# Performance work log

Hardware: AMD Instinct MI355X
Metric: run time of the kernel (lower is better)

Reference implementation:

```python
import jax, jax.numpy as jnp
import numpy as np

B, T, C, H = 2, 2048, 1024, 16
DH = C // H  # 64


def setup_inputs() -> dict:
    key = jax.random.key(0)
    ks = jax.random.split(key, 8)
    scale = 1.0 / np.sqrt(C)
    x = jax.random.normal(ks[0], (B, T, C), dtype=jnp.float32)
    mask = jax.random.randint(ks[1], (B, T), 0, 2, dtype=jnp.int32)
    Wq = jax.random.normal(ks[2], (C, C), dtype=jnp.float32) * scale
    bq = jnp.zeros((C,), dtype=jnp.float32)
    Wk = jax.random.normal(ks[3], (C, C), dtype=jnp.float32) * scale
    bk = jnp.zeros((C,), dtype=jnp.float32)
    Wv = jax.random.normal(ks[4], (C, C), dtype=jnp.float32) * scale
    bv = jnp.zeros((C,), dtype=jnp.float32)
    return {"x": x, "Wq": Wq, "bq": bq, "Wk": Wk, "bk": bk, "Wv": Wv, "bv": bv, "mask": mask}


def reference(x, Wq, bq, Wk, bk, Wv, bv, mask):
    # q/k/v projections: [B,T,C] -> [B,H,T,DH]
    def proj(W, b):
        return (x @ W + b).reshape(B, T, H, DH).transpose(0, 2, 1, 3)

    q = proj(Wq, bq)
    k = proj(Wk, bk)
    v = proj(Wv, bv)

    att = jnp.einsum("bhqd,bhkd->bhqk", q, k) * (1.0 / np.sqrt(DH))

    # outer-product padding mask: square_mask[b,q,k] = mask[b,q]*mask[b,k]
    m = mask.astype(jnp.float32)
    square_mask = m[:, :, None] * m[:, None, :]           # [B,T,T]
    sm = (square_mask != 0)[:, None, :, :]                 # [B,1,T,T]
    att = jnp.where(sm, att, -jnp.inf)

    # rows that are fully masked (query token padded) -> softmax gives NaN
    # in torch; torch then zeros the NaNs. Replicate with a safe softmax.
    row_valid = (mask != 0)[:, None, :, None]              # [B,1,T,1]
    att_safe = jnp.where(row_valid, att, 0.0)
    att = jax.nn.softmax(att_safe, axis=-1)
    att = jnp.where(row_valid, att, 0.0)
    # attn_pdrop = 0.0 -> dropout is identity

    y = jnp.einsum("bhqk,bhkd->bhqd", att, v)              # [B,H,T,DH]
    y = y.transpose(0, 2, 1, 3).reshape(B, T, C)
    return y
```

## Files before the change

### kernel.cpp

```cpp
#include <hip/hip_runtime.h>

#define B_ 2
#define T_ 2048
#define C_ 1024
#define H_ 16
#define DH_ 64

typedef __attribute__((ext_vector_type(8))) _Float16 half8;
typedef __attribute__((ext_vector_type(4))) _Float16 half4;
typedef __attribute__((ext_vector_type(2))) __fp16 fp16x2;
typedef __attribute__((ext_vector_type(4))) float f32x4;
typedef __attribute__((ext_vector_type(16))) float f32x16;

__device__ __forceinline__ unsigned short f2h(float f) {
    union { _Float16 h; unsigned short u; } cv; cv.h = (_Float16)f; return cv.u;
}
__device__ __forceinline__ unsigned pk2(float a, float b) {
    union { fp16x2 h; unsigned u; } cv;
    cv.h = __builtin_amdgcn_cvt_pkrtz(a, b);
    return cv.u;
}
__device__ __forceinline__ void plswap(unsigned &a, unsigned &b) {
    asm volatile("v_permlane32_swap_b32 %0, %1" : "+v"(a), "+v"(b));
}

__device__ __forceinline__ void gll16(const void* g, void* l) {
    __builtin_amdgcn_global_load_lds(
        (const __attribute__((address_space(1))) void*)g,
        (__attribute__((address_space(3))) void*)l, 16, 0, 0);
}

__global__ __launch_bounds__(256) void prep_kernel(
    const float* __restrict__ x, unsigned short* __restrict__ xf,
    const int* __restrict__ mask, unsigned short* __restrict__ mb,
    const float* __restrict__ Wq, const float* __restrict__ Wk,
    const float* __restrict__ Wv, unsigned short* __restrict__ wt)
{
    __shared__ float tile[32][33];
    const int tid = threadIdx.x;

    if (blockIdx.x < 2048) {
        const size_t idx8 = ((size_t)blockIdx.x * 256 + tid) * 8;
        float4 v0 = *(const float4*)(x + idx8);
        float4 v1 = *(const float4*)(x + idx8 + 4);
        float f[8] = {v0.x, v0.y, v0.z, v0.w, v1.x, v1.y, v1.z, v1.w};
        unsigned short h[8];
#pragma unroll
        for (int i = 0; i < 8; i++) h[i] = f2h(f[i]);
        *(uint4*)(xf + idx8) = *(const uint4*)h;

        if (blockIdx.x == 0) {
#pragma unroll
            for (int j = 0; j < 16; j++) {
                int i = tid * 16 + j;
                mb[i] = (mask[i] != 0) ? (unsigned short)0x3C00 : (unsigned short)0;
            }
        }
    } else {
        const int idx = blockIdx.x - 2048;
        const int z   = idx >> 10;
        const int rem = idx & 1023;
        const int n0  = (rem & 31) * 32;
        const int k0  = (rem >> 5) * 32;
        const float* __restrict__ W = (z == 0) ? Wq : (z == 1) ? Wk : Wv;
        unsigned short* __restrict__ wtz = wt + (size_t)z * C_ * C_;
        const int tx = tid & 31;
        const int ty = tid >> 5;
#pragma unroll
        for (int j = 0; j < 4; j++)
            tile[ty + j * 8][tx] = W[(size_t)(k0 + ty + j * 8) * C_ + n0 + tx];
        __syncthreads();
#pragma unroll
        for (int j = 0; j < 4; j++)
            wtz[(size_t)(n0 + ty + j * 8) * C_ + k0 + tx] = f2h(tile[tx][ty + j * 8]);
    }
}

__global__ __launch_bounds__(256) void qkv_mfma_kernel(
    const unsigned short* __restrict__ xf, const unsigned short* __restrict__ wt,
    const float* __restrict__ bq, const float* __restrict__ bk,
    const float* __restrict__ bv, const int* __restrict__ maskp,
    unsigned short* __restrict__ qb, unsigned short* __restrict__ kb,
    unsigned short* __restrict__ vt)
{
    __shared__ unsigned short sX[128 * 64];
    __shared__ unsigned short sW[128 * 64];

    const int bid  = blockIdx.x;
    const int virt = (bid & 7) * 96 + (bid >> 3);
    const int yz   = virt >> 5;
    const int tokb = virt & 31;
    const int z    = yz >> 3;
    const int yb   = yz & 7;

    const float* __restrict__ bias = (z == 0) ? bq : (z == 1) ? bk : bv;
    const unsigned short* __restrict__ wtz = wt + (size_t)z * C_ * C_;

    const int tok0 = tokb * 128;
    const int col0 = yb * 128;
    const int wv    = threadIdx.x >> 6;
    const int lane  = threadIdx.x & 63;
    const int l15   = lane & 15;
    const int quad  = lane >> 4;
    const int l7    = l15 & 7;
    const int wm    = wv >> 1;
    const int wn    = wv & 1;
    const int lrow8 = lane >> 3;
    const int gch   = (lane & 7) ^ lrow8;

    f32x4 acc[4][4];
#pragma unroll
    for (int i = 0; i < 4; i++)
#pragma unroll
        for (int j = 0; j < 4; j++) acc[i][j] = (f32x4){0.f, 0.f, 0.f, 0.f};

    int aoff[4][2], boff[4][2];
#pragma unroll
    for (int i = 0; i < 4; i++)
#pragma unroll
        for (int s = 0; s < 2; s++) {
            aoff[i][s] = (wm * 64 + i * 16 + l15) * 64 + (((s * 4 + quad) ^ l7) * 8);
            boff[i][s] = (wn * 64 + i * 16 + l15) * 64 + (((s * 4 + quad) ^ l7) * 8);
        }

    const unsigned short* Abuf = (z < 2) ? sX : sW;
    const unsigned short* Bbuf = (z < 2) ? sW : sX;

    for (int k0 = 0; k0 < C_; k0 += 64) {
        __syncthreads();
#pragma unroll
        for (int s = 0; s < 8; ++s) {
            int g    = (s << 2) + wv;
            int tsel = g >> 4;
            int r0   = (g & 15) << 3;
            const unsigned short* src = tsel ? wtz : xf;
            unsigned short*       dst = tsel ? sW  : sX;
            int rowg = tsel ? col0 : tok0;
            gll16(src + (size_t)(rowg + r0 + lrow8) * C_ + k0 + gch * 8,
                  dst + r0 * 64);
        }
        __syncthreads();

        half8 af[4][2], bf_[4][2];
#pragma unroll
        for (int i = 0; i < 4; i++)
#pragma unroll
            for (int s = 0; s < 2; s++) {
                af[i][s]  = *(const half8*)&Abuf[aoff[i][s]];
                bf_[i][s] = *(const half8*)&Bbuf[boff[i][s]];
            }
#pragma unroll
        for (int s = 0; s < 2; s++)
#pragma unroll
            for (int j = 0; j < 4; j++)
#pragma unroll
                for (int i = 0; i < 4; i++)
                    acc[i][j] = __builtin_amdgcn_mfma_f32_16x16x32_f16(
                        af[i][s], bf_[j][s], acc[i][j], 0, 0, 0);
    }

    if (z == 0) {
#pragma unroll
        for (int j = 0; j < 4; j++) {
            int col = col0 + wn * 64 + j * 16 + l15;
            int h = col >> 6, d = col & 63;
            float bs = bias[col];
#pragma unroll
            for (int i = 0; i < 4; i++) {
#pragma unroll
                for (int r = 0; r < 4; r++) {
                    int tok = tok0 + wm * 64 + i * 16 + quad * 4 + r;
                    int bidx = tok >> 11, t = tok & (T_ - 1);
                    qb[((size_t)(bidx * H_ + h) * T_ + t) * DH_ + d] =
                        f2h((acc[i][j][r] + bs) * 0.18033688011112042f);
                }
            }
        }
    } else if (z == 1) {
#pragma unroll
        for (int j = 0; j < 4; j++) {
            int col = col0 + wn * 64 + j * 16 + l15;
            int h = col >> 6, d = col & 63;
            float bs = bias[col];
#pragma unroll
            for (int i = 0; i < 4; i++) {
#pragma unroll
                for (int r = 0; r < 4; r++) {
                    int tok = tok0 + wm * 64 + i * 16 + quad * 4 + r;
                    int bidx = tok >> 11, t = tok & (T_ - 1);
                    kb[((size_t)(bidx * H_ + h) * T_ + t) * DH_ + d] =
                        f2h(acc[i][j][r] + bs);
                }
            }
        }
    } else {
        float mv4[4]; int bidx4[4], t4[4];
#pragma unroll
        for (int j = 0; j < 4; j++) {
            int tok = tok0 + wn * 64 + j * 16 + l15;
            bidx4[j] = tok >> 11; t4[j] = tok & (T_ - 1);
            mv4[j] = (maskp[bidx4[j] * T_ + t4[j]] != 0) ? 1.f : 0.f;
        }
#pragma unroll
        for (int i = 0; i < 4; i++) {
#pragma unroll
            for (int r = 0; r < 4; r++) {
                int col = col0 + wm * 64 + i * 16 + quad * 4 + r;
                int h = col >> 6, d = col & 63;
                float bs = bias[col];
#pragma unroll
                for (int j = 0; j < 4; j++) {
                    vt[((size_t)(bidx4[j] * H_ + h) * DH_ + d) * T_ + t4[j]] =
                        f2h((acc[i][j][r] + bs) * mv4[j]);
                }
            }
        }
    }
}

__global__ __launch_bounds__(256, 2) void attn_mfma_kernel(
    const unsigned short* __restrict__ qb,
    const unsigned short* __restrict__ kb,
    const unsigned short* __restrict__ vt,
    const int* __restrict__ mask,
    const unsigned short* __restrict__ mb,
    float* __restrict__ out)
{
    __shared__ unsigned short Ks[2][64 * 64];
    __shared__ unsigned short Vs[2][64 * 64];

    const int bh   = blockIdx.x;
    const int b    = bh >> 4;
    const int h    = bh & 15;
    const int wv   = threadIdx.x >> 6;
    const int lane = threadIdx.x & 63;
    const int l31  = lane & 31;
    const int hi   = lane >> 5;
    const int l7b  = l31 & 7;
    const int q0w  = blockIdx.y * 128 + wv * 32;

    const unsigned short* kbh = kb + (size_t)bh * T_ * DH_;
    const unsigned short* vbh = vt + (size_t)bh * DH_ * T_;
    const unsigned short* mbb = mb + b * T_;
    const int* __restrict__ mrow = mask + b * T_;

    half8 qf[4];
#pragma unroll
    for (int m = 0; m < 4; ++m)
        qf[m] = *(const half8*)(qb + ((size_t)bh * T_ + q0w + l31) * DH_
                                + m * 16 + hi * 8);

    f32x16 o0, o1, lacc;
#pragma unroll
    for (int r = 0; r < 16; ++r) { o0[r] = 0.f; o1[r] = 0.f; lacc[r] = 0.f; }

    const int lrow = lane >> 3;
    const int gch  = (lane & 7) ^ lrow;

#pragma unroll
    for (int s = 0; s < 4; ++s) {
        int j  = (wv << 2) + s;
        int rb = j & 7;
        if (j < 8) gll16(kbh + (size_t)(rb * 8 + lrow) * DH_ + gch * 8, &Ks[0][rb * 512]);
        else       gll16(vbh + (size_t)(rb * 8 + lrow) * T_  + gch * 8, &Vs[0][rb * 512]);
    }

    for (int kt = 0; kt < 32; ++kt) {
        const int cur   = kt & 1;
        const int kbase = kt * 64;
        __syncthreads();

        if (kt < 31) {
            const int nb = kbase + 64;
#pragma unroll
            for (int s = 0; s < 4; ++s) {
                int j  = (wv << 2) + s;
                int rb = j & 7;
                if (j < 8) gll16(kbh + (size_t)(nb + rb * 8 + lrow) * DH_ + gch * 8,
                                 &Ks[cur ^ 1][rb * 512]);
                else       gll16(vbh + (size_t)(rb * 8 + lrow) * T_ + nb + gch * 8,
                                 &Vs[cur ^ 1][rb * 512]);
            }
        }

        const unsigned short* Kc = &Ks[cur][0];
        const unsigned short* Vc = &Vs[cur][0];

        half8 bm[4];
#pragma unroll
        for (int c = 0; c < 4; ++c)
            bm[c] = *(const half8*)(mbb + kbase + c * 16 + hi * 8);

        half8 pa[4];
#pragma unroll
        for (int st = 0; st < 2; ++st) {
            f32x16 sa;
#pragma unroll
            for (int r = 0; r < 16; ++r) sa[r] = 0.f;
#pragma unroll
            for (int m = 0; m < 4; ++m) {
                half8 kf = *(const half8*)(Kc + (st * 32 + l31) * 64
                                           + (((m * 2 + hi) ^ l7b) * 8));
                sa = __builtin_amdgcn_mfma_f32_32x32x16_f16(kf, qf[m], sa, 0, 0, 0);
            }
            float p[16];
#pragma unroll
            for (int r = 0; r < 16; ++r) p[r] = __builtin_amdgcn_exp2f(sa[r]);
#pragma unroll
            for (int kh = 0; kh < 2; ++kh) {
                unsigned w0 = pk2(p[kh * 8 + 0], p[kh * 8 + 1]);
                unsigned w2 = pk2(p[kh * 8 + 4], p[kh * 8 + 5]);
                unsigned w1 = pk2(p[kh * 8 + 2], p[kh * 8 + 3]);
                unsigned w3 = pk2(p[kh * 8 + 6], p[kh * 8 + 7]);
                plswap(w0, w2);
                plswap(w1, w3);
                union { unsigned u[4]; half8 hh; } cv;
                cv.u[0] = w0; cv.u[1] = w1; cv.u[2] = w2; cv.u[3] = w3;
                pa[st * 2 + kh] = cv.hh;
            }
        }

#pragma unroll
        for (int c = 0; c < 4; ++c)
            lacc = __builtin_amdgcn_mfma_f32_32x32x16_f16(pa[c], bm[c], lacc, 0, 0, 0);

#pragma unroll
        for (int c = 0; c < 4; ++c) {
            half8 v0 = *(const half8*)(Vc + (l31) * 64      + (((c * 2 + hi) ^ l7b) * 8));
            half8 v1 = *(const half8*)(Vc + (32 + l31) * 64 + (((c * 2 + hi) ^ l7b) * 8));
            o0 = __builtin_amdgcn_mfma_f32_32x32x16_f16(pa[c], v0, o0, 0, 0, 0);
            o1 = __builtin_amdgcn_mfma_f32_32x32x16_f16(pa[c], v1, o1, 0, 0, 0);
        }
    }

#pragma unroll
    for (int r = 0; r < 16; ++r) {
        int q = q0w + (r & 3) + 8 * (r >> 2) + 4 * hi;
        float lv = lacc[r];
        float iv = (mrow[q] != 0 && lv > 0.f) ? (1.0f / lv) : 0.f;
        float* orow = out + ((size_t)(b * T_ + q)) * C_ + h * DH_;
        orow[l31]      = o0[r] * iv;
        orow[32 + l31] = o1[r] * iv;
    }
}

extern "C" void kernel_launch(void* const* d_in, const int* in_sizes, int n_in,
                              void* d_out, int out_size, void* d_ws, size_t ws_size,
                              hipStream_t stream)
{
    (void)in_sizes; (void)n_in; (void)out_size; (void)ws_size;
    const float* x  = (const float*)d_in[0];
    const float* Wq = (const float*)d_in[1];
    const float* bq = (const float*)d_in[2];
    const float* Wk = (const float*)d_in[3];
    const float* bk = (const float*)d_in[4];
    const float* Wv = (const float*)d_in[5];
    const float* bv = (const float*)d_in[6];
    const int* mask = (const int*)d_in[7];
    float* out = (float*)d_out;

    const size_t NX = (size_t)B_ * T_ * C_;
    unsigned short* xf = (unsigned short*)d_ws;
    unsigned short* wt = xf + NX;
    unsigned short* qb = wt + (size_t)3 * C_ * C_;
    unsigned short* kb = qb + NX;
    unsigned short* vt = kb + NX;
    unsigned short* mb = vt + NX;

    prep_kernel<<<5120, 256, 0, stream>>>(x, xf, mask, mb, Wq, Wk, Wv, wt);
    qkv_mfma_kernel<<<768, 256, 0, stream>>>(
        xf, wt, bq, bk, bv, mask, qb, kb, vt);
    attn_mfma_kernel<<<dim3(32, 16), 256, 0, stream>>>(qb, kb, vt, mask, mb, out);
}
```

Measured before the change: 170.9 us.

## Double-buffer QKV GEMM LDS tiles and remap blocks for XCD locality

The QKV projection GEMM now keeps two LDS buffers for the X and W tiles. It issues the global-to-LDS load for the next k-slice before running the MFMAs on the current one, so load latency overlaps compute and one barrier per iteration is dropped. The block-to-tile mapping is also changed so that each XCD handles a contiguous 8-token-block by 12-column-block region, which should improve L2 reuse of shared X rows and W columns. The cost is twice the LDS per block, which may reduce occupancy.

```diff
diff --git a/kernel.cpp b/kernel.cpp
--- a/kernel.cpp
+++ b/kernel.cpp
@@ -83,13 +83,16 @@
     unsigned short* __restrict__ qb, unsigned short* __restrict__ kb,
     unsigned short* __restrict__ vt)
 {
-    __shared__ unsigned short sX[128 * 64];
-    __shared__ unsigned short sW[128 * 64];
+    __shared__ unsigned short sX[2][128 * 64];
+    __shared__ unsigned short sW[2][128 * 64];
 
     const int bid  = blockIdx.x;
-    const int virt = (bid & 7) * 96 + (bid >> 3);
-    const int yz   = virt >> 5;
-    const int tokb = virt & 31;
+    const int xcd  = bid & 7;
+    const int idx  = bid >> 3;
+    const int tokl = idx / 12;
+    const int yzl  = idx % 12;
+    const int tokb = (xcd >> 1) * 8 + tokl;
+    const int yz   = (xcd & 1) * 12 + yzl;
     const int z    = yz >> 3;
     const int yb   = yz & 7;
 
@@ -123,23 +126,29 @@
             boff[i][s] = (wn * 64 + i * 16 + l15) * 64 + (((s * 4 + quad) ^ l7) * 8);
         }
 
-    const unsigned short* Abuf = (z < 2) ? sX : sW;
-    const unsigned short* Bbuf = (z < 2) ? sW : sX;
+#define STAGE_QKV(k0v, bi) do {                                               \
+    _Pragma("unroll")                                                         \
+    for (int s = 0; s < 8; ++s) {                                             \
+        int g    = (s << 2) + wv;                                             \
+        int tsel = g >> 4;                                                    \
+        int r0   = (g & 15) << 3;                                             \
+        const unsigned short* src = tsel ? wtz : xf;                          \
+        unsigned short*       dst = tsel ? &sW[bi][0] : &sX[bi][0];           \
+        int rowg = tsel ? col0 : tok0;                                        \
+        gll16(src + (size_t)(rowg + r0 + lrow8) * C_ + (k0v) + gch * 8,       \
+              dst + r0 * 64);                                                 \
+    }                                                                         \
+} while (0)
+
+    STAGE_QKV(0, 0);
 
     for (int k0 = 0; k0 < C_; k0 += 64) {
+        const int cur = (k0 >> 6) & 1;
         __syncthreads();
-#pragma unroll
-        for (int s = 0; s < 8; ++s) {
-            int g    = (s << 2) + wv;
-            int tsel = g >> 4;
-            int r0   = (g & 15) << 3;
-            const unsigned short* src = tsel ? wtz : xf;
-            unsigned short*       dst = tsel ? sW  : sX;
-            int rowg = tsel ? col0 : tok0;
-            gll16(src + (size_t)(rowg + r0 + lrow8) * C_ + k0 + gch * 8,
-                  dst + r0 * 64);
-        }
-        __syncthreads();
+        if (k0 + 64 < C_) STAGE_QKV(k0 + 64, cur ^ 1);
+
+        const unsigned short* Abuf = (z < 2) ? &sX[cur][0] : &sW[cur][0];
+        const unsigned short* Bbuf = (z < 2) ? &sW[cur][0] : &sX[cur][0];
 
         half8 af[4][2], bf_[4][2];
 #pragma unroll
@@ -158,6 +167,7 @@
                     acc[i][j] = __builtin_amdgcn_mfma_f32_16x16x32_f16(
                         af[i][s], bf_[j][s], acc[i][j], 0, 0, 0);
     }
+#undef STAGE_QKV
 
     if (z == 0) {
 #pragma unroll
```

After: 167.3 us. 2.1% less time.
